# Kernel tuning notes

Hardware: AMD Instinct MI355X
Metric: run time of the kernel (lower is better)

## Reference

```python
import jax, jax.numpy as jnp
import numpy as np

N, E, IN, HID, H, L, G = 20000, 320000, 128, 64, 4, 3, 128

def setup_inputs() -> dict:
    key = jax.random.key(0)
    ks = jax.random.split(key, 14)
    x = jax.random.normal(ks[0], (N, IN), dtype=jnp.float32)
    edge_index = jax.random.randint(ks[1], (2, E), 0, N, dtype=jnp.int64)
    batch = jnp.sort(jax.random.randint(ks[2], (N,), 0, G, dtype=jnp.int64))
    s_in = 1.0 / np.sqrt(IN)
    s_h = 1.0 / np.sqrt(HID)
    lin_W = jax.random.normal(ks[3], (IN, HID), jnp.float32) * s_in
    lin_b = jax.random.normal(ks[4], (HID,), jnp.float32) * 0.02
    Wq = jax.random.normal(ks[5], (L, HID, H * HID), jnp.float32) * s_h
    bq = jax.random.normal(ks[6], (L, H * HID), jnp.float32) * 0.02
    Wk = jax.random.normal(ks[7], (L, HID, H * HID), jnp.float32) * s_h
    bk = jax.random.normal(ks[8], (L, H * HID), jnp.float32) * 0.02
    Wv = jax.random.normal(ks[9], (L, HID, H * HID), jnp.float32) * s_h
    bv = jax.random.normal(ks[10], (L, H * HID), jnp.float32) * 0.02
    Ws = jax.random.normal(ks[11], (L, HID, HID), jnp.float32) * s_h
    bs = jax.random.normal(ks[12], (L, HID), jnp.float32) * 0.02
    return {"x": x, "edge_index": edge_index, "batch": batch,
            "lin_W": lin_W, "lin_b": lin_b, "Wq": Wq, "bq": bq,
            "Wk": Wk, "bk": bk, "Wv": Wv, "bv": bv, "Ws": Ws, "bs": bs}

def _transformer_conv(h, src, dst, Wq, bq, Wk, bk, Wv, bv, Ws, bs):
    # PyG TransformerConv(hid, hid, heads=H, concat=False), beta=False, root_weight=True
    n = h.shape[0]
    C = HID  # per-head dim
    q = (h @ Wq + bq).reshape(n, H, C)
    k = (h @ Wk + bk).reshape(n, H, C)
    v = (h @ Wv + bv).reshape(n, H, C)
    # per-edge attention logits: q_i . k_j / sqrt(C), i=dst (target), j=src
    alpha = jnp.einsum('ehc,ehc->eh', q[dst], k[src]) * (1.0 / np.sqrt(C))  # [E,H]
    # segment softmax over edges grouped by target node
    amax = jax.ops.segment_max(alpha, dst, num_segments=n)  # [N,H]
    amax = jnp.where(jnp.isfinite(amax), amax, 0.0)
    ex = jnp.exp(alpha - amax[dst])
    denom = jax.ops.segment_sum(ex, dst, num_segments=n)
    a = ex / jnp.maximum(denom[dst], 1e-16)  # [E,H]
    msg = a[:, :, None] * v[src]  # [E,H,C]
    agg = jax.ops.segment_sum(msg.reshape(-1, H * C), dst, num_segments=n)
    out = agg.reshape(n, H, C).mean(axis=1)  # concat=False -> head mean
    return out + h @ Ws + bs  # root/skip connection

def reference(x, edge_index, batch, lin_W, lin_b, Wq, bq, Wk, bk, Wv, bv, Ws, bs):
    src, dst = edge_index[0], edge_index[1]
    h = x @ lin_W + lin_b  # [N, HID]; dropout inactive in eval
    for l in range(L):
        h = jax.nn.relu(_transformer_conv(h, src, dst, Wq[l], bq[l], Wk[l], bk[l],
                                          Wv[l], bv[l], Ws[l], bs[l]))
    # global_add_pool: sum node features per graph
    return jax.ops.segment_sum(h, batch, num_segments=G)  # [G, HID]
```

## Files before the change

kernel.cpp:

```cpp
#include <hip/hip_runtime.h>
#include <math.h>

#define N_NODES 20000
#define N_EDGES 320000
#define DIM_IN 128
#define HID 64
#define HEADS 4
#define LAYERS 3
#define GRAPHS 128
#define QSS 320

typedef unsigned short ushort;
typedef ushort ushort8 __attribute__((ext_vector_type(8)));
typedef ushort ushort4v __attribute__((ext_vector_type(4)));
typedef short short8 __attribute__((ext_vector_type(8)));
typedef float f32x4 __attribute__((ext_vector_type(4)));

__device__ __forceinline__ float bf2f(ushort u) {
    return __uint_as_float(((unsigned int)u) << 16);
}
__device__ __forceinline__ ushort f2bf(float f) {
    unsigned int b = __float_as_uint(f);
    return (ushort)((b + 0x7FFFu + ((b >> 16) & 1u)) >> 16);
}


__global__ void hist_kernel(const int* __restrict__ dst, int* __restrict__ counts, int n) {
    int e = blockIdx.x * 256 + threadIdx.x;
    if (e < n) atomicAdd(&counts[dst[e]], 1);
}

__global__ __launch_bounds__(256) void blocksum_kernel(const int* __restrict__ counts,
                                                       int* __restrict__ bsum, int n) {
    int i = blockIdx.x * 256 + threadIdx.x;
    int v = (i < n) ? counts[i] : 0;
    int lane = threadIdx.x & 63, wave = threadIdx.x >> 6;
#pragma unroll
    for (int off = 32; off >= 1; off >>= 1) v += __shfl_xor(v, off);
    __shared__ int ws[4];
    if (lane == 0) ws[wave] = v;
    __syncthreads();
    if (threadIdx.x == 0) bsum[blockIdx.x] = ws[0] + ws[1] + ws[2] + ws[3];
}

__global__ __launch_bounds__(128) void scanb_kernel(const int* __restrict__ bsum,
                                                    int* __restrict__ bexcl, int nb) {
    int tid = threadIdx.x;
    int v = (tid < nb) ? bsum[tid] : 0;
    int lane = tid & 63, wave = tid >> 6;
    int s = v;
#pragma unroll
    for (int off = 1; off < 64; off <<= 1) {
        int t = __shfl_up(s, off);
        if (lane >= off) s += t;
    }
    __shared__ int w0sum;
    if (tid == 63) w0sum = s;
    __syncthreads();
    int excl = s - v + (wave ? w0sum : 0);
    if (tid < nb) bexcl[tid] = excl;
}

__global__ __launch_bounds__(256) void expand_kernel(const int* __restrict__ counts,
                                                     const int* __restrict__ bexcl,
                                                     int* __restrict__ offs,
                                                     int* __restrict__ cursor, int n) {
    int i = blockIdx.x * 256 + threadIdx.x;
    int v = (i < n) ? counts[i] : 0;
    int lane = threadIdx.x & 63, wave = threadIdx.x >> 6;
    int s = v;
#pragma unroll
    for (int off = 1; off < 64; off <<= 1) {
        int t = __shfl_up(s, off);
        if (lane >= off) s += t;
    }
    __shared__ int wsum[4];
    if (lane == 63) wsum[wave] = s;
    __syncthreads();
    int add = bexcl[blockIdx.x];
    for (int w = 0; w < wave; ++w) add += wsum[w];
    int excl = add + s - v;
    if (i < n) { offs[i] = excl; cursor[i] = excl; }
    if (i == 0) offs[n] = N_EDGES;
}

__global__ void scatter_kernel(const int* __restrict__ src, const int* __restrict__ dst,
                               int* __restrict__ cursor, int* __restrict__ csr, int n) {
    int e = blockIdx.x * 256 + threadIdx.x;
    if (e < n) {
        int d = dst[e];
        int pos = atomicAdd(&cursor[d], 1);
        csr[pos] = src[e];
    }
}


__global__ __launch_bounds__(256) void wcvt_all_kernel(
        const float* __restrict__ Wq, const float* __restrict__ bq,
        const float* __restrict__ Wk, const float* __restrict__ bk,
        const float* __restrict__ Wv, const float* __restrict__ bv,
        const float* __restrict__ Ws, const float* __restrict__ bs,
        const float* __restrict__ linW,
        ushort* __restrict__ Wt3, float* __restrict__ bias3,
        ushort* __restrict__ Wlt) {
    const int PER = 832 * 64;
    int idx = blockIdx.x * 256 + threadIdx.x;
    if (idx < 3 * PER) {
        int l = idx / PER;
        int r = idx - l * PER;
        int j = r >> 6, k = r & 63;
        const float* Wq_l = Wq + (size_t)l * HID * 256;
        const float* Wk_l = Wk + (size_t)l * HID * 256;
        const float* Wv_l = Wv + (size_t)l * HID * 256;
        const float* Ws_l = Ws + (size_t)l * HID * 64;
        float w;
        if (j < 256) {
            w = Wq_l[(size_t)k * 256 + j];
        } else if (j < 768) {
            int pout = j - 256;
            int isv = (pout >> 2) & 1;
            int low2 = pout & 3;
            int g = pout >> 3;
            int srccol = (g >> 4) * 64 + (g & 15) * 4 + low2;
            w = isv ? Wv_l[(size_t)k * 256 + srccol] : Wk_l[(size_t)k * 256 + srccol];
        } else {
            w = Ws_l[(size_t)k * 64 + (j - 768)];
        }
        Wt3[idx] = f2bf(w);
    } else {
        int idx2 = idx - 3 * PER;
        if (idx2 < 64 * DIM_IN) {
            int col = idx2 >> 7, k = idx2 & 127;
            Wlt[idx2] = f2bf(linW[(size_t)k * HID + col]);
        }
    }
    if (idx < 3 * 832) {
        int l = idx / 832, j = idx - l * 832;
        float b;
        if (j < 256) {
            b = bq[l * 256 + j];
        } else if (j < 768) {
            int pout = j - 256;
            int isv = (pout >> 2) & 1;
            int low2 = pout & 3;
            int g = pout >> 3;
            int srccol = (g >> 4) * 64 + (g & 15) * 4 + low2;
            b = isv ? bv[l * 256 + srccol] : bk[l * 256 + srccol];
        } else {
            b = bs[l * 64 + (j - 768)];
        }
        bias3[idx] = b;
    }
}


__global__ __launch_bounds__(256) void lin_kernel(const float* __restrict__ x,
                                                  const ushort* __restrict__ Wlt,
                                                  const float* __restrict__ lb,
                                                  float* __restrict__ h0) {
    int tid = threadIdx.x;
    int w = tid >> 6, l = tid & 63;
    int r0 = blockIdx.x * 64 + w * 16;
    int row = r0 + (l & 15);
    int rowc = (row < N_NODES) ? row : (N_NODES - 1);

    short8 a[4];
#pragma unroll
    for (int kc = 0; kc < 4; ++kc) {
        const float* xp = x + (size_t)rowc * DIM_IN + kc * 32 + (l >> 4) * 8;
        float4 f0 = *(const float4*)xp;
        float4 f1 = *(const float4*)(xp + 4);
        ushort8 u;
        u[0] = f2bf(f0.x); u[1] = f2bf(f0.y); u[2] = f2bf(f0.z); u[3] = f2bf(f0.w);
        u[4] = f2bf(f1.x); u[5] = f2bf(f1.y); u[6] = f2bf(f1.z); u[7] = f2bf(f1.w);
        a[kc] = __builtin_bit_cast(short8, u);
    }

    f32x4 acc[4];
#pragma unroll
    for (int t = 0; t < 4; ++t) acc[t] = (f32x4){0.f, 0.f, 0.f, 0.f};

    const ushort* wb = Wlt + (size_t)(l & 15) * DIM_IN + (l >> 4) * 8;
#pragma unroll
    for (int t = 0; t < 4; ++t) {
#pragma unroll
        for (int kc = 0; kc < 4; ++kc) {
            short8 b = *(const short8*)(wb + (size_t)t * 16 * DIM_IN + kc * 32);
            acc[t] = __builtin_amdgcn_mfma_f32_16x16x32_bf16(b, a[kc], acc[t], 0, 0, 0);
        }
    }

    if (row < N_NODES) {
#pragma unroll
        for (int t = 0; t < 4; ++t) {
            int j = t * 16 + ((l >> 4) << 2);
            float4 bias = *(const float4*)(lb + j);
            float4 o;
            o.x = acc[t][0] + bias.x;
            o.y = acc[t][1] + bias.y;
            o.z = acc[t][2] + bias.z;
            o.w = acc[t][3] + bias.w;
            *(float4*)(h0 + (size_t)row * HID + j) = o;
        }
    }
}


__global__ __launch_bounds__(512) void proj_kernel(const float* __restrict__ h,
                                                   const ushort* __restrict__ Wt,
                                                   const float* __restrict__ bias_cat,
                                                   float* __restrict__ qs,
                                                   ushort* __restrict__ kvpack) {
    int tid = threadIdx.x;
    int w = tid >> 6, l = tid & 63;
    int r0 = blockIdx.x * 32 + (w & 1) * 16;
    int c0 = (w >> 1) * 208;
    int row = r0 + (l & 15);
    int koff = (l >> 4) * 8;

    short8 a[2];
#pragma unroll
    for (int m = 0; m < 2; ++m) {
        const float* hp = h + (size_t)row * HID + m * 32 + koff;
        float4 f0 = *(const float4*)hp;
        float4 f1 = *(const float4*)(hp + 4);
        ushort8 u;
        u[0] = f2bf(f0.x); u[1] = f2bf(f0.y); u[2] = f2bf(f0.z); u[3] = f2bf(f0.w);
        u[4] = f2bf(f1.x); u[5] = f2bf(f1.y); u[6] = f2bf(f1.z); u[7] = f2bf(f1.w);
        a[m] = __builtin_bit_cast(short8, u);
    }

    f32x4 acc[13];
#pragma unroll
    for (int t = 0; t < 13; ++t) acc[t] = (f32x4){0.f, 0.f, 0.f, 0.f};

    const ushort* wb = Wt + ((size_t)(c0 + (l & 15))) * HID + koff;
#pragma unroll
    for (int t = 0; t < 13; ++t) {
        short8 b0 = *(const short8*)(wb + (size_t)t * 16 * HID);
        short8 b1 = *(const short8*)(wb + (size_t)t * 16 * HID + 32);
        acc[t] = __builtin_amdgcn_mfma_f32_16x16x32_bf16(b0, a[0], acc[t], 0, 0, 0);
        acc[t] = __builtin_amdgcn_mfma_f32_16x16x32_bf16(b1, a[1], acc[t], 0, 0, 0);
    }

#pragma unroll
    for (int t = 0; t < 13; ++t) {
        int j = c0 + t * 16 + ((l >> 4) << 2);
        float4 bias = *(const float4*)(bias_cat + j);
        float4 o;
        o.x = acc[t][0] + bias.x;
        o.y = acc[t][1] + bias.y;
        o.z = acc[t][2] + bias.z;
        o.w = acc[t][3] + bias.w;
        if (j < 256) {
            *(float4*)(qs + (size_t)row * QSS + j) = o;
        } else if (j < 768) {
            int pout = j - 256;
            ushort4v u4;
            u4[0] = f2bf(o.x); u4[1] = f2bf(o.y); u4[2] = f2bf(o.z); u4[3] = f2bf(o.w);
            *(ushort4v*)(kvpack + (size_t)row * 512 + pout) = u4;
        } else {
            *(float4*)(qs + (size_t)row * QSS + 256 + (j - 768)) = o;
        }
    }
}


__global__ __launch_bounds__(256) void edge_kernel(const float* __restrict__ qs,
                                                   const ushort8* __restrict__ kvp,
                                                   const int* __restrict__ offs,
                                                   const int* __restrict__ csr,
                                                   float* __restrict__ hout) {
    int wave = threadIdx.x >> 6;
    int lane = threadIdx.x & 63;
    int node = blockIdx.x * 4 + wave;
    if (node >= N_NODES) return;
    int hh = lane >> 4;
    int cb = (lane & 15) * 4;

    const float* nb = qs + (size_t)node * QSS;
    float4 q = *(const float4*)(nb + hh * 64 + cb);

    const float SCL = 0.125f * 1.44269504088896340736f;

    float m = -INFINITY, l = 0.f;
    float4 acc = make_float4(0.f, 0.f, 0.f, 0.f);

    int e0 = offs[node], e1 = offs[node + 1];
    int cnt = e1 - e0;

    ushort8 cur = (ushort8)(0);
    ushort8 nxt = (ushort8)(0);
    if (cnt > 0) cur = kvp[(size_t)csr[e0] * 64 + lane];
    if (cnt > 1) nxt = kvp[(size_t)csr[e0 + 1] * 64 + lane];

    for (int i = 0; i < cnt; ++i) {
        ushort8 u = cur;
        cur = nxt;
        if (i + 2 < cnt) nxt = kvp[(size_t)csr[e0 + i + 2] * 64 + lane];

        float p = q.x * bf2f(u[0]) + q.y * bf2f(u[1]) + q.z * bf2f(u[2]) + q.w * bf2f(u[3]);
        p += __shfl_xor(p, 1);
        p += __shfl_xor(p, 2);
        p += __shfl_xor(p, 4);
        p += __shfl_xor(p, 8);
        float alpha = p * SCL;
        if (__any(alpha > m)) {
            float nm = fmaxf(m, alpha);
            float sc = exp2f(m - nm);
            l *= sc; acc.x *= sc; acc.y *= sc; acc.z *= sc; acc.w *= sc;
            m = nm;
        }
        float pe = exp2f(alpha - m);
        l += pe;
        acc.x += pe * bf2f(u[4]);
        acc.y += pe * bf2f(u[5]);
        acc.z += pe * bf2f(u[6]);
        acc.w += pe * bf2f(u[7]);
    }

    float inv = (l > 0.f) ? (1.f / l) : 0.f;
    float4 r;
    r.x = acc.x * inv;
    r.y = acc.y * inv;
    r.z = acc.z * inv;
    r.w = acc.w * inv;
    r.x += __shfl_xor(r.x, 16); r.x += __shfl_xor(r.x, 32);
    r.y += __shfl_xor(r.y, 16); r.y += __shfl_xor(r.y, 32);
    r.z += __shfl_xor(r.z, 16); r.z += __shfl_xor(r.z, 32);
    r.w += __shfl_xor(r.w, 16); r.w += __shfl_xor(r.w, 32);

    if (hh == 0) {
        float4 s = *(const float4*)(nb + 256 + cb);
        float4 o;
        o.x = fmaxf(r.x * 0.25f + s.x, 0.f);
        o.y = fmaxf(r.y * 0.25f + s.y, 0.f);
        o.z = fmaxf(r.z * 0.25f + s.z, 0.f);
        o.w = fmaxf(r.w * 0.25f + s.w, 0.f);
        *(float4*)(hout + (size_t)node * HID + cb) = o;
    }
}


__global__ __launch_bounds__(256) void pool_kernel(const float* __restrict__ h,
                                                   const int* __restrict__ batch,
                                                   float* __restrict__ out) {
    int g = blockIdx.x;
    int lo = 0, hi = N_NODES;
    while (lo < hi) { int mid = (lo + hi) >> 1; if (batch[mid] < g) lo = mid + 1; else hi = mid; }
    int start = lo;
    hi = N_NODES;
    while (lo < hi) { int mid = (lo + hi) >> 1; if (batch[mid] < g + 1) lo = mid + 1; else hi = mid; }
    int end = lo;
    int c = threadIdx.x & 63;
    int sub = threadIdx.x >> 6;
    float acc = 0.f;
    for (int i = start + sub; i < end; i += 4) acc += h[(size_t)i * HID + c];
    __shared__ float lds[4][64];
    lds[sub][c] = acc;
    __syncthreads();
    if (sub == 0) out[g * HID + c] = lds[0][c] + lds[1][c] + lds[2][c] + lds[3][c];
}


extern "C" void kernel_launch(void* const* d_in, const int* in_sizes, int n_in,
                              void* d_out, int out_size, void* d_ws, size_t ws_size,
                              hipStream_t stream) {
    const float* x    = (const float*)d_in[0];
    const int*   edge = (const int*)d_in[1];
    const int*   batch= (const int*)d_in[2];
    const float* linW = (const float*)d_in[3];
    const float* linb = (const float*)d_in[4];
    const float* Wq   = (const float*)d_in[5];
    const float* bq   = (const float*)d_in[6];
    const float* Wk   = (const float*)d_in[7];
    const float* bk   = (const float*)d_in[8];
    const float* Wv   = (const float*)d_in[9];
    const float* bv   = (const float*)d_in[10];
    const float* Ws   = (const float*)d_in[11];
    const float* bs   = (const float*)d_in[12];
    float* out = (float*)d_out;

    const int* src = edge;
    const int* dst = edge + N_EDGES;

    float* h0  = (float*)d_ws;
    float* h1  = h0 + (size_t)N_NODES * HID;
    float* qs  = h1 + (size_t)N_NODES * HID;
    ushort* kvpack = (ushort*)(qs + (size_t)N_NODES * QSS);
    int* counts = (int*)(kvpack + (size_t)N_NODES * 512);
    int* offs   = counts + N_NODES;
    int* cursor = offs + N_NODES + 1;
    int* csr    = cursor + N_NODES;
    int* bsum   = csr + N_EDGES;
    int* bexcl  = bsum + 128;
    ushort* Wt3 = (ushort*)(bexcl + 128);
    float* bias3 = (float*)(Wt3 + 3 * 832 * 64);
    ushort* Wlt = (ushort*)(bias3 + 3 * 832);

    const int NB = (N_NODES + 255) / 256;

    hipMemsetAsync(counts, 0, N_NODES * sizeof(int), stream);
    hist_kernel<<<(N_EDGES + 255) / 256, 256, 0, stream>>>(dst, counts, N_EDGES);
    blocksum_kernel<<<NB, 256, 0, stream>>>(counts, bsum, N_NODES);
    scanb_kernel<<<1, 128, 0, stream>>>(bsum, bexcl, NB);
    expand_kernel<<<NB, 256, 0, stream>>>(counts, bexcl, offs, cursor, N_NODES);
    scatter_kernel<<<(N_EDGES + 255) / 256, 256, 0, stream>>>(src, dst, cursor, csr, N_EDGES);

    wcvt_all_kernel<<<(3 * 832 * 64 + 64 * DIM_IN + 255) / 256, 256, 0, stream>>>(
        Wq, bq, Wk, bk, Wv, bv, Ws, bs, linW, Wt3, bias3, Wlt);

    lin_kernel<<<(N_NODES + 63) / 64, 256, 0, stream>>>(x, Wlt, linb, h0);

    float* hc = h0;
    float* hn = h1;
    for (int l = 0; l < LAYERS; ++l) {
        proj_kernel<<<N_NODES / 32, 512, 0, stream>>>(hc,
            Wt3 + (size_t)l * 832 * 64, bias3 + (size_t)l * 832, qs, kvpack);
        edge_kernel<<<N_NODES / 4, 256, 0, stream>>>(qs, (const ushort8*)kvpack, offs, csr, hn);
        float* t = hc; hc = hn; hn = t;
    }

    pool_kernel<<<GRAPHS, 256, 0, stream>>>(hc, batch, out);
}
```

Before: 406.7 us.

## Fuse projection into preceding edge/linear kernels and store q/skip in bf16

Each layer's q/k/v/skip projection is folded into the end of the previous kernel: the input linear layer feeds layer 0's projection through LDS, and each attention kernel computes the next layer's projection for its 16 nodes. The separate proj kernels disappear, along with the round trip of h through global memory. q and the skip term are now stored as bf16 instead of fp32, which halves their traffic but costs some precision. The changes also add double-buffered qs/kv buffers and a __syncthreads per block, and attention blocks now carry extra MFMA work that may affect occupancy.

```diff
diff --git a/kernel.cpp b/kernel.cpp
--- a/kernel.cpp
+++ b/kernel.cpp
@@ -8,7 +8,7 @@
 #define HEADS 4
 #define LAYERS 3
 #define GRAPHS 128
-#define QSS 320
+#define HOP 68
 
 typedef unsigned short ushort;
 typedef ushort ushort8 __attribute__((ext_vector_type(8)));
@@ -154,10 +154,55 @@
 }
 
 
-__global__ __launch_bounds__(256) void lin_kernel(const float* __restrict__ x,
-                                                  const ushort* __restrict__ Wlt,
-                                                  const float* __restrict__ lb,
-                                                  float* __restrict__ h0) {
+__device__ __forceinline__ void proj_rows(const float* __restrict__ ho,
+        const ushort* __restrict__ Wt, const float* __restrict__ bias_cat,
+        ushort* __restrict__ qsb, ushort* __restrict__ kvp,
+        int r0, int lane, int t0, int tstep) {
+    int lr = lane & 15;
+    int grow = r0 + lr;
+    int koff = (lane >> 4) * 8;
+    short8 bh[2];
+#pragma unroll
+    for (int mm = 0; mm < 2; ++mm) {
+        const float* hp = ho + lr * HOP + mm * 32 + koff;
+        float4 f0 = *(const float4*)hp;
+        float4 f1 = *(const float4*)(hp + 4);
+        ushort8 u;
+        u[0] = f2bf(f0.x); u[1] = f2bf(f0.y); u[2] = f2bf(f0.z); u[3] = f2bf(f0.w);
+        u[4] = f2bf(f1.x); u[5] = f2bf(f1.y); u[6] = f2bf(f1.z); u[7] = f2bf(f1.w);
+        bh[mm] = __builtin_bit_cast(short8, u);
+    }
+    bool ok = (grow < N_NODES);
+    for (int t = t0; t < 52; t += tstep) {
+        const ushort* wb = Wt + (size_t)(t * 16 + lr) * HID + koff;
+        short8 w0 = *(const short8*)wb;
+        short8 w1 = *(const short8*)(wb + 32);
+        f32x4 a_ = (f32x4){0.f, 0.f, 0.f, 0.f};
+        a_ = __builtin_amdgcn_mfma_f32_16x16x32_bf16(w0, bh[0], a_, 0, 0, 0);
+        a_ = __builtin_amdgcn_mfma_f32_16x16x32_bf16(w1, bh[1], a_, 0, 0, 0);
+        int j = t * 16 + ((lane >> 4) << 2);
+        float4 bs4 = *(const float4*)(bias_cat + j);
+        ushort4v u4;
+        u4[0] = f2bf(a_[0] + bs4.x);
+        u4[1] = f2bf(a_[1] + bs4.y);
+        u4[2] = f2bf(a_[2] + bs4.z);
+        u4[3] = f2bf(a_[3] + bs4.w);
+        if (ok) {
+            ushort* dst;
+            if (j < 256)      dst = qsb + (size_t)grow * 320 + j;
+            else if (j < 768) dst = kvp + (size_t)grow * 512 + (j - 256);
+            else              dst = qsb + (size_t)grow * 320 + 256 + (j - 768);
+            *(ushort4v*)dst = u4;
+        }
+    }
+}
+
+
+__global__ __launch_bounds__(256) void linproj_kernel(const float* __restrict__ x,
+        const ushort* __restrict__ Wlt, const float* __restrict__ lb,
+        const ushort* __restrict__ Wt0, const float* __restrict__ bias0,
+        ushort* __restrict__ qsb, ushort* __restrict__ kvp) {
+    __shared__ float ho[64 * HOP];
     int tid = threadIdx.x;
     int w = tid >> 6, l = tid & 63;
     int r0 = blockIdx.x * 64 + w * 16;
@@ -190,99 +235,32 @@
         }
     }
 
-    if (row < N_NODES) {
-#pragma unroll
-        for (int t = 0; t < 4; ++t) {
-            int j = t * 16 + ((l >> 4) << 2);
-            float4 bias = *(const float4*)(lb + j);
-            float4 o;
-            o.x = acc[t][0] + bias.x;
-            o.y = acc[t][1] + bias.y;
-            o.z = acc[t][2] + bias.z;
-            o.w = acc[t][3] + bias.w;
-            *(float4*)(h0 + (size_t)row * HID + j) = o;
-        }
-    }
-}
-
-
-__global__ __launch_bounds__(512) void proj_kernel(const float* __restrict__ h,
-                                                   const ushort* __restrict__ Wt,
-                                                   const float* __restrict__ bias_cat,
-                                                   float* __restrict__ qs,
-                                                   ushort* __restrict__ kvpack) {
-    int tid = threadIdx.x;
-    int w = tid >> 6, l = tid & 63;
-    int r0 = blockIdx.x * 32 + (w & 1) * 16;
-    int c0 = (w >> 1) * 208;
-    int row = r0 + (l & 15);
-    int koff = (l >> 4) * 8;
-
-    short8 a[2];
-#pragma unroll
-    for (int m = 0; m < 2; ++m) {
-        const float* hp = h + (size_t)row * HID + m * 32 + koff;
-        float4 f0 = *(const float4*)hp;
-        float4 f1 = *(const float4*)(hp + 4);
-        ushort8 u;
-        u[0] = f2bf(f0.x); u[1] = f2bf(f0.y); u[2] = f2bf(f0.z); u[3] = f2bf(f0.w);
-        u[4] = f2bf(f1.x); u[5] = f2bf(f1.y); u[6] = f2bf(f1.z); u[7] = f2bf(f1.w);
-        a[m] = __builtin_bit_cast(short8, u);
-    }
-
-    f32x4 acc[13];
-#pragma unroll
-    for (int t = 0; t < 13; ++t) acc[t] = (f32x4){0.f, 0.f, 0.f, 0.f};
-
-    const ushort* wb = Wt + ((size_t)(c0 + (l & 15))) * HID + koff;
-#pragma unroll
-    for (int t = 0; t < 13; ++t) {
-        short8 b0 = *(const short8*)(wb + (size_t)t * 16 * HID);
-        short8 b1 = *(const short8*)(wb + (size_t)t * 16 * HID + 32);
-        acc[t] = __builtin_amdgcn_mfma_f32_16x16x32_bf16(b0, a[0], acc[t], 0, 0, 0);
-        acc[t] = __builtin_amdgcn_mfma_f32_16x16x32_bf16(b1, a[1], acc[t], 0, 0, 0);
-    }
-
-#pragma unroll
-    for (int t = 0; t < 13; ++t) {
-        int j = c0 + t * 16 + ((l >> 4) << 2);
-        float4 bias = *(const float4*)(bias_cat + j);
+    float* hrow = ho + (size_t)(w * 16 + (l & 15)) * HOP;
+#pragma unroll
+    for (int t = 0; t < 4; ++t) {
+        int j = t * 16 + ((l >> 4) << 2);
+        float4 bias = *(const float4*)(lb + j);
         float4 o;
         o.x = acc[t][0] + bias.x;
         o.y = acc[t][1] + bias.y;
         o.z = acc[t][2] + bias.z;
         o.w = acc[t][3] + bias.w;
-        if (j < 256) {
-            *(float4*)(qs + (size_t)row * QSS + j) = o;
-        } else if (j < 768) {
-            int pout = j - 256;
-            ushort4v u4;
-            u4[0] = f2bf(o.x); u4[1] = f2bf(o.y); u4[2] = f2bf(o.z); u4[3] = f2bf(o.w);
-            *(ushort4v*)(kvpack + (size_t)row * 512 + pout) = u4;
-        } else {
-            *(float4*)(qs + (size_t)row * QSS + 256 + (j - 768)) = o;
-        }
-    }
-}
-
-
-__global__ __launch_bounds__(256) void edge_kernel(const float* __restrict__ qs,
-                                                   const ushort8* __restrict__ kvp,
-                                                   const int* __restrict__ offs,
-                                                   const int* __restrict__ csr,
-                                                   float* __restrict__ hout) {
-    int wave = threadIdx.x >> 6;
-    int lane = threadIdx.x & 63;
-    int node = blockIdx.x * 4 + wave;
-    if (node >= N_NODES) return;
+        *(float4*)(hrow + j) = o;
+    }
+    proj_rows(ho + (size_t)w * 16 * HOP, Wt0, bias0, qsb, kvp, r0, l, 0, 1);
+}
+
+
+__device__ __forceinline__ float4 attn_node(int node, int lane,
+        const ushort* __restrict__ qsb, const ushort8* __restrict__ kvp,
+        const int* __restrict__ offs, const int* __restrict__ csr) {
     int hh = lane >> 4;
     int cb = (lane & 15) * 4;
-
-    const float* nb = qs + (size_t)node * QSS;
-    float4 q = *(const float4*)(nb + hh * 64 + cb);
+    const ushort* nb = qsb + (size_t)node * 320;
+    ushort4v qu = *(const ushort4v*)(nb + hh * 64 + cb);
+    float qx = bf2f(qu[0]), qy = bf2f(qu[1]), qz = bf2f(qu[2]), qw = bf2f(qu[3]);
 
     const float SCL = 0.125f * 1.44269504088896340736f;
-
     float m = -INFINITY, l = 0.f;
     float4 acc = make_float4(0.f, 0.f, 0.f, 0.f);
 
@@ -299,7 +277,7 @@
         cur = nxt;
         if (i + 2 < cnt) nxt = kvp[(size_t)csr[e0 + i + 2] * 64 + lane];
 
-        float p = q.x * bf2f(u[0]) + q.y * bf2f(u[1]) + q.z * bf2f(u[2]) + q.w * bf2f(u[3]);
+        float p = qx * bf2f(u[0]) + qy * bf2f(u[1]) + qz * bf2f(u[2]) + qw * bf2f(u[3]);
         p += __shfl_xor(p, 1);
         p += __shfl_xor(p, 2);
         p += __shfl_xor(p, 4);
@@ -330,15 +308,46 @@
     r.z += __shfl_xor(r.z, 16); r.z += __shfl_xor(r.z, 32);
     r.w += __shfl_xor(r.w, 16); r.w += __shfl_xor(r.w, 32);
 
-    if (hh == 0) {
-        float4 s = *(const float4*)(nb + 256 + cb);
-        float4 o;
-        o.x = fmaxf(r.x * 0.25f + s.x, 0.f);
-        o.y = fmaxf(r.y * 0.25f + s.y, 0.f);
-        o.z = fmaxf(r.z * 0.25f + s.z, 0.f);
-        o.w = fmaxf(r.w * 0.25f + s.w, 0.f);
-        *(float4*)(hout + (size_t)node * HID + cb) = o;
-    }
+    ushort4v su = *(const ushort4v*)(nb + 256 + cb);
+    float4 o;
+    o.x = fmaxf(r.x * 0.25f + bf2f(su[0]), 0.f);
+    o.y = fmaxf(r.y * 0.25f + bf2f(su[1]), 0.f);
+    o.z = fmaxf(r.z * 0.25f + bf2f(su[2]), 0.f);
+    o.w = fmaxf(r.w * 0.25f + bf2f(su[3]), 0.f);
+    return o;
+}
+
+
+__global__ __launch_bounds__(512) void edgeproj_kernel(const ushort* __restrict__ qsb_in,
+        const ushort8* __restrict__ kvp_in,
+        const int* __restrict__ offs, const int* __restrict__ csr,
+        const ushort* __restrict__ Wt_next, const float* __restrict__ bias_next,
+        ushort* __restrict__ qsb_out, ushort* __restrict__ kvp_out) {
+    __shared__ float ho[16 * HOP];
+    int tid = threadIdx.x;
+    int w = tid >> 6, l = tid & 63;
+    int nbase = blockIdx.x * 16 + w * 2;
+#pragma unroll
+    for (int nd = 0; nd < 2; ++nd) {
+        int node = nbase + nd;
+        float4 o = attn_node(node, l, qsb_in, kvp_in, offs, csr);
+        if ((l >> 4) == 0)
+            *(float4*)(ho + (size_t)(w * 2 + nd) * HOP + (l & 15) * 4) = o;
+    }
+    __syncthreads();
+    proj_rows(ho, Wt_next, bias_next, qsb_out, kvp_out, blockIdx.x * 16, l, w, 8);
+}
+
+
+__global__ __launch_bounds__(256) void edge_kernel(const ushort* __restrict__ qsb,
+        const ushort8* __restrict__ kvp,
+        const int* __restrict__ offs, const int* __restrict__ csr,
+        float* __restrict__ hout) {
+    int w = threadIdx.x >> 6, l = threadIdx.x & 63;
+    int node = blockIdx.x * 4 + w;
+    float4 o = attn_node(node, l, qsb, kvp, offs, csr);
+    if ((l >> 4) == 0)
+        *(float4*)(hout + (size_t)node * HID + (l & 15) * 4) = o;
 }
 
 
@@ -384,11 +393,12 @@
     const int* src = edge;
     const int* dst = edge + N_EDGES;
 
-    float* h0  = (float*)d_ws;
-    float* h1  = h0 + (size_t)N_NODES * HID;
-    float* qs  = h1 + (size_t)N_NODES * HID;
-    ushort* kvpack = (ushort*)(qs + (size_t)N_NODES * QSS);
-    int* counts = (int*)(kvpack + (size_t)N_NODES * 512);
+    ushort* qsb0 = (ushort*)d_ws;
+    ushort* qsb1 = qsb0 + (size_t)N_NODES * 320;
+    ushort* kvp0 = qsb1 + (size_t)N_NODES * 320;
+    ushort* kvp1 = kvp0 + (size_t)N_NODES * 512;
+    float*  h3   = (float*)kvp1;
+    int* counts = (int*)(kvp1 + (size_t)N_NODES * 512);
     int* offs   = counts + N_NODES;
     int* cursor = offs + N_NODES + 1;
     int* csr    = cursor + N_NODES;
@@ -410,16 +420,19 @@
     wcvt_all_kernel<<<(3 * 832 * 64 + 64 * DIM_IN + 255) / 256, 256, 0, stream>>>(
         Wq, bq, Wk, bk, Wv, bv, Ws, bs, linW, Wt3, bias3, Wlt);
 
-    lin_kernel<<<(N_NODES + 63) / 64, 256, 0, stream>>>(x, Wlt, linb, h0);
-
-    float* hc = h0;
-    float* hn = h1;
-    for (int l = 0; l < LAYERS; ++l) {
-        proj_kernel<<<N_NODES / 32, 512, 0, stream>>>(hc,
-            Wt3 + (size_t)l * 832 * 64, bias3 + (size_t)l * 832, qs, kvpack);
-        edge_kernel<<<N_NODES / 4, 256, 0, stream>>>(qs, (const ushort8*)kvpack, offs, csr, hn);
-        float* t = hc; hc = hn; hn = t;
-    }
-
-    pool_kernel<<<GRAPHS, 256, 0, stream>>>(hc, batch, out);
-}
+    linproj_kernel<<<(N_NODES + 63) / 64, 256, 0, stream>>>(
+        x, Wlt, linb, Wt3, bias3, qsb0, kvp0);
+
+    edgeproj_kernel<<<N_NODES / 16, 512, 0, stream>>>(
+        qsb0, (const ushort8*)kvp0, offs, csr,
+        Wt3 + (size_t)1 * 832 * 64, bias3 + 832, qsb1, kvp1);
+
+    edgeproj_kernel<<<N_NODES / 16, 512, 0, stream>>>(
+        qsb1, (const ushort8*)kvp1, offs, csr,
+        Wt3 + (size_t)2 * 832 * 64, bias3 + 1664, qsb0, kvp0);
+
+    edge_kernel<<<N_NODES / 4, 256, 0, stream>>>(
+        qsb0, (const ushort8*)kvp0, offs, csr, h3);
+
+    pool_kernel<<<GRAPHS, 256, 0, stream>>>(h3, batch, out);
+}
```

After: 407.9 us. No clear change (+0.3%).
